# Performance work log

Measured on AMD Instinct MI355X. Metric: run time of the kernel, lower is better.

Reference implementation:

```python
import jax, jax.numpy as jnp
import numpy as np
from jax.ops import segment_sum, segment_max

N, E = 50000, 500000
D_IN, D_H, D_OUT = 128, 256, 40
BN_EPS = 1e-5


def setup_inputs() -> dict:
    key = jax.random.key(0)
    ks = jax.random.split(key, 16)
    g = lambda k, shape, fan: jax.random.normal(k, shape, jnp.float32) * (1.0 / np.sqrt(fan))
    inp = {
        "x": jax.random.normal(ks[0], (N, D_IN), jnp.float32),
        "edge_index": jax.random.randint(ks[1], (2, E), 0, N, jnp.int64),
        # GAT (heads=1)
        "W_gat": g(ks[2], (D_IN, D_H), D_IN),
        "att_src": g(ks[3], (D_H,), D_H),
        "att_dst": g(ks[4], (D_H,), D_H),
        "b_gat": jnp.zeros((D_H,), jnp.float32),
        # GIN MLP
        "W_gin1": g(ks[5], (D_IN, D_H), D_IN),
        "b_gin1": jnp.zeros((D_H,), jnp.float32),
        "W_gin2": g(ks[6], (D_H, D_H), D_H),
        "b_gin2": jnp.zeros((D_H,), jnp.float32),
        # GCN
        "W_gcn": g(ks[7], (D_IN, D_H), D_IN),
        "b_gcn": jnp.zeros((D_H,), jnp.float32),
        # BatchNorm1d(3*hidden)
        "gamma": jnp.ones((3 * D_H,), jnp.float32),
        "beta": jnp.zeros((3 * D_H,), jnp.float32),
        # head
        "W_lin": g(ks[8], (3 * D_H, D_H), 3 * D_H),
        "b_lin": jnp.zeros((D_H,), jnp.float32),
        "W_lin2": g(ks[9], (D_H, D_OUT), D_H),
        "b_lin2": jnp.zeros((D_OUT,), jnp.float32),
    }
    return inp


def _forward(x, edge_index, W_gat, att_src, att_dst, b_gat, W_gin1, b_gin1,
             W_gin2, b_gin2, W_gcn, b_gcn, gamma, beta, W_lin, b_lin, W_lin2, b_lin2):
    n = x.shape[0]
    src, dst = edge_index[0], edge_index[1]
    loop = jnp.arange(n, dtype=src.dtype)
    src_sl = jnp.concatenate([src, loop])  # edges + self-loops (GAT/GCN)
    dst_sl = jnp.concatenate([dst, loop])

    # ---- GATConv (1 head), messages src -> dst, softmax over dst ----
    xs = x @ W_gat                                   # [N, H]
    a = jax.nn.leaky_relu(xs @ att_src, negative_slope=0.2) if False else None
    e = (xs @ att_src)[src_sl] + (xs @ att_dst)[dst_sl]   # [E+N]
    e = jax.nn.leaky_relu(e, negative_slope=0.2)
    m = segment_max(e, dst_sl, num_segments=n)
    w = jnp.exp(e - m[dst_sl])
    denom = segment_sum(w, dst_sl, num_segments=n)
    alpha = w / denom[dst_sl]
    x_gat = segment_sum(alpha[:, None] * xs[src_sl], dst_sl, num_segments=n) + b_gat

    # ---- GINConv (eps=0): MLP(x + sum_neighbors x_j) ----
    agg = segment_sum(x[src], dst, num_segments=n)
    h = x + agg
    x_gin = jax.nn.relu(h @ W_gin1 + b_gin1) @ W_gin2 + b_gin2

    # ---- GCNConv: symmetric normalization with self-loops ----
    deg = segment_sum(jnp.ones_like(dst_sl, dtype=x.dtype), dst_sl, num_segments=n)
    dis = jax.lax.rsqrt(jnp.maximum(deg, 1.0))  # deg >= 1 due to self-loops
    norm = dis[src_sl] * dis[dst_sl]
    xw = x @ W_gcn
    x_gcn = segment_sum(norm[:, None] * xw[src_sl], dst_sl, num_segments=n) + b_gcn

    # ---- concat -> BN (training-mode batch stats) -> ReLU -> MLP head ----
    xc = jnp.concatenate([x_gat, x_gin, x_gcn], axis=1)  # [N, 3H]
    mu = jnp.mean(xc, axis=0)
    var = jnp.mean((xc - mu) ** 2, axis=0)
    xb = (xc - mu) * jax.lax.rsqrt(var + BN_EPS) * gamma + beta
    h2 = jax.nn.relu(jax.nn.relu(xb) @ W_lin + b_lin)
    return h2 @ W_lin2 + b_lin2


def reference(x, edge_index, W_gat, att_src, att_dst, b_gat, W_gin1, b_gin1,
              W_gin2, b_gin2, W_gcn, b_gcn, gamma, beta, W_lin, b_lin, W_lin2, b_lin2):
    return _forward(x, edge_index, W_gat, att_src, att_dst, b_gat, W_gin1, b_gin1,
                    W_gin2, b_gin2, W_gcn, b_gcn, gamma, beta, W_lin, b_lin, W_lin2, b_lin2)
```

## Files before the change

kernel.cpp:

```cpp
#include <hip/hip_runtime.h>
#include <math.h>

#define NN 50000
#define NE 500000

typedef __attribute__((ext_vector_type(8))) short short8;
typedef __attribute__((ext_vector_type(4))) float f32x4;

__device__ __forceinline__ float leaky02(float x) { return x > 0.f ? x : 0.2f * x; }
__device__ __forceinline__ ushort f2b(float f) {
    uint u = __float_as_uint(f);
    u += 0x7fffu + ((u >> 16) & 1u);
    return (ushort)(u >> 16);
}
__device__ __forceinline__ float b2f(ushort h) { return __uint_as_float(((uint)h) << 16); }
__device__ __forceinline__ float b2f_lo(uint w) { return __uint_as_float(w << 16); }
__device__ __forceinline__ float b2f_hi(uint w) { return __uint_as_float(w & 0xffff0000u); }
__device__ __forceinline__ uint pack2(float a, float b) {
    return (uint)f2b(a) | ((uint)f2b(b) << 16);
}

__global__ void mm_wt(const float* __restrict__ W, ushort* __restrict__ Wt, int K, int Nc)
{
    int idx = blockIdx.x * 256 + threadIdx.x;
    if (idx >= K * Nc) return;
    int n = idx / K, k = idx - n * K;
    Wt[idx] = f2b(W[(size_t)k * Nc + n]);
}

__global__ void mm_attvec(const float* __restrict__ W, const float* __restrict__ as_,
                          const float* __restrict__ ad_, float* __restrict__ va, float* __restrict__ vd)
{
    int i = threadIdx.x;
    const float* vec = (i < 128) ? as_ : ad_;
    int k = i & 127;
    float s = 0.f;
    for (int j = 0; j < 256; ++j) s += W[(size_t)k * 256 + j] * vec[j];
    if (i < 128) va[k] = s; else vd[k] = s;
}

__global__ __launch_bounds__(256) void mm_cvt_es(const float* __restrict__ x,
                                                 const float* __restrict__ va, const float* __restrict__ vd,
                                                 ushort* __restrict__ xb,
                                                 float* __restrict__ es, float* __restrict__ ed)
{
    int node = blockIdx.x * 4 + (threadIdx.x >> 6);
    int lane = threadIdx.x & 63;
    if (node >= NN) return;
    float2 xv = *(const float2*)(x + (size_t)node * 128 + lane * 2);
    float2 a = *(const float2*)(va + lane * 2);
    float2 b = *(const float2*)(vd + lane * 2);
    *(uint*)(xb + (size_t)node * 128 + lane * 2) = pack2(xv.x, xv.y);
    float s = xv.x * a.x + xv.y * a.y;
    float d = xv.x * b.x + xv.y * b.y;
    #pragma unroll
    for (int off = 32; off; off >>= 1) {
        s += __shfl_down(s, off);
        d += __shfl_down(d, off);
    }
    if (lane == 0) { es[node] = s; ed[node] = d; }
}

__global__ void mm_count(const int* __restrict__ dst, int* __restrict__ deg)
{
    int e = blockIdx.x * 256 + threadIdx.x;
    if (e >= NE) return;
    atomicAdd(&deg[dst[e]], 1);
}

__global__ __launch_bounds__(256) void mm_scan1(const int* __restrict__ deg, int* __restrict__ part)
{
    __shared__ int red[256];
    int i = blockIdx.x * 256 + threadIdx.x;
    red[threadIdx.x] = (i < NN) ? deg[i] : 0;
    __syncthreads();
    for (int off = 128; off; off >>= 1) {
        if (threadIdx.x < off) red[threadIdx.x] += red[threadIdx.x + off];
        __syncthreads();
    }
    if (threadIdx.x == 0) part[blockIdx.x] = red[0];
}

__global__ __launch_bounds__(256) void mm_scan2(int* __restrict__ part, int nb)
{
    __shared__ int tile[256];
    int t = threadIdx.x;
    int v = (t < nb) ? part[t] : 0;
    tile[t] = v; __syncthreads();
    for (int off = 1; off < 256; off <<= 1) {
        int a = (t >= off) ? tile[t - off] : 0;
        __syncthreads();
        tile[t] += a;
        __syncthreads();
    }
    if (t < nb) part[t] = tile[t] - v;
}

__global__ __launch_bounds__(256) void mm_scan3(const int* __restrict__ deg, const int* __restrict__ part,
                                                int* __restrict__ row_ptr, int* __restrict__ cursor)
{
    __shared__ int tile[256];
    int t = threadIdx.x;
    int i = blockIdx.x * 256 + t;
    int v = (i < NN) ? deg[i] : 0;
    tile[t] = v; __syncthreads();
    for (int off = 1; off < 256; off <<= 1) {
        int a = (t >= off) ? tile[t - off] : 0;
        __syncthreads();
        tile[t] += a;
        __syncthreads();
    }
    if (i < NN) {
        int ex = part[blockIdx.x] + tile[t] - v;
        row_ptr[i] = ex;
        cursor[i] = ex;
    }
    if (i == 0) row_ptr[NN] = NE;
}

__global__ void mm_fill(const int* __restrict__ src, const int* __restrict__ dst,
                        int* __restrict__ cursor, int* __restrict__ csr_src)
{
    int e = blockIdx.x * 256 + threadIdx.x;
    if (e >= NE) return;
    int pos = atomicAdd(&cursor[dst[e]], 1);
    csr_src[pos] = src[e];
}

__global__ void mm_dis(const int* __restrict__ row_ptr, float* __restrict__ dis)
{
    int i = blockIdx.x * 256 + threadIdx.x;
    if (i >= NN) return;
    dis[i] = rsqrtf((float)(row_ptr[i + 1] - row_ptr[i] + 1));
}

__global__ __launch_bounds__(256) void mm_node_agg(
    const int* __restrict__ row_ptr, const int* __restrict__ csr_src,
    const float* __restrict__ es, const float* __restrict__ ed,
    const float* __restrict__ dis,
    const ushort* __restrict__ xb, ushort* __restrict__ aggb)
{
    int d = blockIdx.x * 4 + (threadIdx.x >> 6);
    int lane = threadIdx.x & 63;
    if (d >= NN) return;
    int start = row_ptr[d], end = row_ptr[d + 1];
    float edd = ed[d], disd = dis[d];
    float selfv = leaky02(es[d] + edd);

    int myidx = -1; float myl = -3.0e38f, mynw = 0.f;
    if (start + lane < end) {
        myidx = csr_src[start + lane];
        myl = leaky02(es[myidx] + edd);
        mynw = dis[myidx] * disd;
    }
    float lmax = fmaxf(selfv, myl);
    for (int e = start + 64 + lane; e < end; e += 64)
        lmax = fmaxf(lmax, leaky02(es[csr_src[e]] + edd));
    #pragma unroll
    for (int off = 1; off < 64; off <<= 1) lmax = fmaxf(lmax, __shfl_xor(lmax, off));
    float m = lmax;

    float lsum = (myidx >= 0) ? __expf(myl - m) : 0.f;
    if (lane == 0) lsum += __expf(selfv - m);
    for (int e = start + 64 + lane; e < end; e += 64)
        lsum += __expf(leaky02(es[csr_src[e]] + edd) - m);
    #pragma unroll
    for (int off = 1; off < 64; off <<= 1) lsum += __shfl_xor(lsum, off);
    float inv = 1.f / lsum;
    float myal = __expf(myl - m) * inv;

    float aself = __expf(selfv - m) * inv;
    float d2 = disd * disd;
    uint wself = *(const uint*)(xb + (size_t)d * 128 + lane * 2);
    float x0 = b2f_lo(wself), x1 = b2f_hi(wself);
    float gat0 = aself * x0, gat1 = aself * x1;
    float gin0 = x0, gin1 = x1;
    float gcn0 = d2 * x0, gcn1 = d2 * x1;

    for (int base = start; base < end; base += 64) {
        int cnt = min(64, end - base);
        int bidx; float bal, bnw;
        if (base == start) { bidx = myidx; bal = myal; bnw = mynw; }
        else {
            bidx = -1; bal = 0.f; bnw = 0.f;
            if (base + lane < end) {
                bidx = csr_src[base + lane];
                bal = __expf(leaky02(es[bidx] + edd) - m) * inv;
                bnw = dis[bidx] * disd;
            }
        }
        int j = 0;
        for (; j + 4 <= cnt; j += 4) {
            int   s0 = __shfl(bidx, j),     s1 = __shfl(bidx, j + 1);
            int   s2 = __shfl(bidx, j + 2), s3 = __shfl(bidx, j + 3);
            float a0 = __shfl(bal, j),      a1 = __shfl(bal, j + 1);
            float a2 = __shfl(bal, j + 2),  a3 = __shfl(bal, j + 3);
            float n0 = __shfl(bnw, j),      n1 = __shfl(bnw, j + 1);
            float n2 = __shfl(bnw, j + 2),  n3 = __shfl(bnw, j + 3);
            uint w0 = *(const uint*)(xb + (size_t)s0 * 128 + lane * 2);
            uint w1 = *(const uint*)(xb + (size_t)s1 * 128 + lane * 2);
            uint w2 = *(const uint*)(xb + (size_t)s2 * 128 + lane * 2);
            uint w3 = *(const uint*)(xb + (size_t)s3 * 128 + lane * 2);
            float p0, p1;
            p0 = b2f_lo(w0); p1 = b2f_hi(w0);
            gat0 += a0 * p0; gat1 += a0 * p1; gin0 += p0; gin1 += p1; gcn0 += n0 * p0; gcn1 += n0 * p1;
            p0 = b2f_lo(w1); p1 = b2f_hi(w1);
            gat0 += a1 * p0; gat1 += a1 * p1; gin0 += p0; gin1 += p1; gcn0 += n1 * p0; gcn1 += n1 * p1;
            p0 = b2f_lo(w2); p1 = b2f_hi(w2);
            gat0 += a2 * p0; gat1 += a2 * p1; gin0 += p0; gin1 += p1; gcn0 += n2 * p0; gcn1 += n2 * p1;
            p0 = b2f_lo(w3); p1 = b2f_hi(w3);
            gat0 += a3 * p0; gat1 += a3 * p1; gin0 += p0; gin1 += p1; gcn0 += n3 * p0; gcn1 += n3 * p1;
        }
        for (; j < cnt; ++j) {
            int   s0 = __shfl(bidx, j);
            float a0 = __shfl(bal, j);
            float n0 = __shfl(bnw, j);
            uint w0 = *(const uint*)(xb + (size_t)s0 * 128 + lane * 2);
            float p0 = b2f_lo(w0), p1 = b2f_hi(w0);
            gat0 += a0 * p0; gat1 += a0 * p1; gin0 += p0; gin1 += p1; gcn0 += n0 * p0; gcn1 += n0 * p1;
        }
    }
    ushort* orow = aggb + (size_t)d * 384;
    *(uint*)(orow + lane * 2)       = pack2(gat0, gat1);
    *(uint*)(orow + 128 + lane * 2) = pack2(gin0, gin1);
    *(uint*)(orow + 256 + lane * 2) = pack2(gcn0, gcn1);
}

__global__ __launch_bounds__(256) void mm_gemm_bf(
    const ushort* __restrict__ A, int lda, const ushort* __restrict__ Bt,
    const float* __restrict__ bias,
    ushort* __restrict__ Cb, int ldc,
    int M, int K, int relu)
{
    __shared__ ushort lds[8192];
    const int tid = threadIdx.x;
    const int wave = tid >> 6, lane = tid & 63;
    const int row0 = blockIdx.x * 128;
    const int col0 = blockIdx.y * 128;

    int arow0 = min(row0 + wave * 16 + (lane >> 2), M - 1);
    int arow1 = min(row0 + 64 + wave * 16 + (lane >> 2), M - 1);
    int brow0 = col0 + wave * 16 + (lane >> 2);
    int brow1 = col0 + 64 + wave * 16 + (lane >> 2);
    const ushort* pa0 = A + (size_t)arow0 * lda + (lane & 3) * 8;
    const ushort* pa1 = A + (size_t)arow1 * lda + (lane & 3) * 8;
    const ushort* pb0 = Bt + (size_t)brow0 * K + (lane & 3) * 8;
    const ushort* pb1 = Bt + (size_t)brow1 * K + (lane & 3) * 8;

    ushort* As = lds;
    ushort* Bs = lds + 4096;
    const int wr = (wave >> 1) * 64, wc = (wave & 1) * 64;

    f32x4 zero = {0.f, 0.f, 0.f, 0.f};
    f32x4 acc[4][4];
    #pragma unroll
    for (int m = 0; m < 4; ++m)
        #pragma unroll
        for (int n = 0; n < 4; ++n) acc[m][n] = zero;

    for (int k0 = 0; k0 < K; k0 += 32) {
        __builtin_amdgcn_global_load_lds((const __attribute__((address_space(1))) void*)pa0,
            (__attribute__((address_space(3))) void*)(As + wave * 512), 16, 0, 0);
        __builtin_amdgcn_global_load_lds((const __attribute__((address_space(1))) void*)pa1,
            (__attribute__((address_space(3))) void*)(As + 2048 + wave * 512), 16, 0, 0);
        __builtin_amdgcn_global_load_lds((const __attribute__((address_space(1))) void*)pb0,
            (__attribute__((address_space(3))) void*)(Bs + wave * 512), 16, 0, 0);
        __builtin_amdgcn_global_load_lds((const __attribute__((address_space(1))) void*)pb1,
            (__attribute__((address_space(3))) void*)(Bs + 2048 + wave * 512), 16, 0, 0);
        pa0 += 32; pa1 += 32; pb0 += 32; pb1 += 32;
        __syncthreads();

        short8 a[4], b[4];
        #pragma unroll
        for (int m = 0; m < 4; ++m)
            a[m] = *(const short8*)&As[(wr + m * 16 + (lane & 15)) * 32 + (lane >> 4) * 8];
        #pragma unroll
        for (int n = 0; n < 4; ++n)
            b[n] = *(const short8*)&Bs[(wc + n * 16 + (lane & 15)) * 32 + (lane >> 4) * 8];
        #pragma unroll
        for (int m = 0; m < 4; ++m)
            #pragma unroll
            for (int n = 0; n < 4; ++n)
                acc[m][n] = __builtin_amdgcn_mfma_f32_16x16x32_bf16(a[m], b[n], acc[m][n], 0, 0, 0);
        __syncthreads();
    }

    #pragma unroll
    for (int n = 0; n < 4; ++n) {
        int col = col0 + wc + n * 16 + (lane & 15);
        float bb = bias ? bias[col] : 0.f;
        #pragma unroll
        for (int m = 0; m < 4; ++m) {
            int rb = row0 + wr + m * 16 + (lane >> 4) * 4;
            #pragma unroll
            for (int r = 0; r < 4; ++r) {
                int row = rb + r;
                if (row < M) {
                    float v = acc[m][n][r] + bb;
                    if (relu) v = fmaxf(v, 0.f);
                    Cb[(size_t)row * ldc + col] = f2b(v);
                }
            }
        }
    }
}

__global__ __launch_bounds__(256) void mm_gemm_bn(
    const ushort* __restrict__ A, const ushort* __restrict__ Bt,
    const float* __restrict__ bias,
    const float* __restrict__ sc, const float* __restrict__ sh,
    ushort* __restrict__ Cb, int ldc, int M)
{
    const int K = 768, lda = 768;
    __shared__ ushort lds[8192];
    const int tid = threadIdx.x;
    const int wave = tid >> 6, lane = tid & 63;
    const int row0 = blockIdx.x * 128;
    const int col0 = blockIdx.y * 128;

    int arow0 = min(row0 + wave * 16 + (lane >> 2), M - 1);
    int arow1 = min(row0 + 64 + wave * 16 + (lane >> 2), M - 1);
    int brow0 = col0 + wave * 16 + (lane >> 2);
    int brow1 = col0 + 64 + wave * 16 + (lane >> 2);
    const ushort* pa0 = A + (size_t)arow0 * lda + (lane & 3) * 8;
    const ushort* pa1 = A + (size_t)arow1 * lda + (lane & 3) * 8;
    const ushort* pb0 = Bt + (size_t)brow0 * K + (lane & 3) * 8;
    const ushort* pb1 = Bt + (size_t)brow1 * K + (lane & 3) * 8;

    ushort* As = lds;
    ushort* Bs = lds + 4096;
    const int wr = (wave >> 1) * 64, wc = (wave & 1) * 64;

    f32x4 zero = {0.f, 0.f, 0.f, 0.f};
    f32x4 acc[4][4];
    #pragma unroll
    for (int m = 0; m < 4; ++m)
        #pragma unroll
        for (int n = 0; n < 4; ++n) acc[m][n] = zero;

    for (int k0 = 0; k0 < K; k0 += 32) {
        __builtin_amdgcn_global_load_lds((const __attribute__((address_space(1))) void*)pb0,
            (__attribute__((address_space(3))) void*)(Bs + wave * 512), 16, 0, 0);
        __builtin_amdgcn_global_load_lds((const __attribute__((address_space(1))) void*)pb1,
            (__attribute__((address_space(3))) void*)(Bs + 2048 + wave * 512), 16, 0, 0);
        uint4 w0 = *(const uint4*)pa0;
        uint4 w1 = *(const uint4*)pa1;
        int c = k0 + (lane & 3) * 8;
        float4 sc0 = *(const float4*)(sc + c), sc1 = *(const float4*)(sc + c + 4);
        float4 sh0 = *(const float4*)(sh + c), sh1 = *(const float4*)(sh + c + 4);
        uint o0x = pack2(fmaxf(b2f_lo(w0.x) * sc0.x + sh0.x, 0.f), fmaxf(b2f_hi(w0.x) * sc0.y + sh0.y, 0.f));
        uint o0y = pack2(fmaxf(b2f_lo(w0.y) * sc0.z + sh0.z, 0.f), fmaxf(b2f_hi(w0.y) * sc0.w + sh0.w, 0.f));
        uint o0z = pack2(fmaxf(b2f_lo(w0.z) * sc1.x + sh1.x, 0.f), fmaxf(b2f_hi(w0.z) * sc1.y + sh1.y, 0.f));
        uint o0w = pack2(fmaxf(b2f_lo(w0.w) * sc1.z + sh1.z, 0.f), fmaxf(b2f_hi(w0.w) * sc1.w + sh1.w, 0.f));
        uint o1x = pack2(fmaxf(b2f_lo(w1.x) * sc0.x + sh0.x, 0.f), fmaxf(b2f_hi(w1.x) * sc0.y + sh0.y, 0.f));
        uint o1y = pack2(fmaxf(b2f_lo(w1.y) * sc0.z + sh0.z, 0.f), fmaxf(b2f_hi(w1.y) * sc0.w + sh0.w, 0.f));
        uint o1z = pack2(fmaxf(b2f_lo(w1.z) * sc1.x + sh1.x, 0.f), fmaxf(b2f_hi(w1.z) * sc1.y + sh1.y, 0.f));
        uint o1w = pack2(fmaxf(b2f_lo(w1.w) * sc1.z + sh1.z, 0.f), fmaxf(b2f_hi(w1.w) * sc1.w + sh1.w, 0.f));
        uint4 oa = {o0x, o0y, o0z, o0w};
        uint4 ob = {o1x, o1y, o1z, o1w};
        *(uint4*)(As + wave * 512 + lane * 8) = oa;
        *(uint4*)(As + 2048 + wave * 512 + lane * 8) = ob;
        pa0 += 32; pa1 += 32; pb0 += 32; pb1 += 32;
        __syncthreads();

        short8 a[4], b[4];
        #pragma unroll
        for (int m = 0; m < 4; ++m)
            a[m] = *(const short8*)&As[(wr + m * 16 + (lane & 15)) * 32 + (lane >> 4) * 8];
        #pragma unroll
        for (int n = 0; n < 4; ++n)
            b[n] = *(const short8*)&Bs[(wc + n * 16 + (lane & 15)) * 32 + (lane >> 4) * 8];
        #pragma unroll
        for (int m = 0; m < 4; ++m)
            #pragma unroll
            for (int n = 0; n < 4; ++n)
                acc[m][n] = __builtin_amdgcn_mfma_f32_16x16x32_bf16(a[m], b[n], acc[m][n], 0, 0, 0);
        __syncthreads();
    }

    #pragma unroll
    for (int n = 0; n < 4; ++n) {
        int col = col0 + wc + n * 16 + (lane & 15);
        float bb = bias[col];
        #pragma unroll
        for (int m = 0; m < 4; ++m) {
            int rb = row0 + wr + m * 16 + (lane >> 4) * 4;
            #pragma unroll
            for (int r = 0; r < 4; ++r) {
                int row = rb + r;
                if (row < M)
                    Cb[(size_t)row * ldc + col] = f2b(fmaxf(acc[m][n][r] + bb, 0.f));
            }
        }
    }
}

__global__ __launch_bounds__(384) void mm_bn_partial(const ushort* __restrict__ xcb, float* __restrict__ sums)
{
    int r0 = blockIdx.x * 128;
    int rend = min(r0 + 128, NN);
    int t = threadIdx.x;
    float s0 = 0, q0 = 0, s1 = 0, q1 = 0;
    for (int r = r0; r < rend; ++r) {
        uint w = *(const uint*)(xcb + (size_t)r * 768 + 2 * t);
        float v0 = b2f_lo(w), v1 = b2f_hi(w);
        s0 += v0; q0 += v0 * v0;
        s1 += v1; q1 += v1 * v1;
    }
    unsafeAtomicAdd(&sums[2 * t], s0);
    unsafeAtomicAdd(&sums[2 * t + 1], s1);
    unsafeAtomicAdd(&sums[768 + 2 * t], q0);
    unsafeAtomicAdd(&sums[768 + 2 * t + 1], q1);
}

__global__ void mm_bn_fin(const float* __restrict__ sums, const float* __restrict__ gamma,
                          const float* __restrict__ beta,
                          float* __restrict__ scale, float* __restrict__ shift)
{
    int c = blockIdx.x * 256 + threadIdx.x;
    if (c >= 768) return;
    float inv = 1.f / (float)NN;
    float mu = sums[c] * inv;
    float ex2 = sums[768 + c] * inv;
    float var = fmaxf(ex2 - mu * mu, 0.f);
    float rs = rsqrtf(var + 1e-5f);
    float sc = gamma[c] * rs;
    scale[c] = sc;
    shift[c] = beta[c] - mu * sc;
}

__global__ __launch_bounds__(256) void mm_head2(const ushort* __restrict__ h2b, const float* __restrict__ W2,
                                                const float* __restrict__ b2, float* __restrict__ out)
{
    __shared__ float Ws[256 * 40];
    for (int i = threadIdx.x; i < 256 * 40; i += 256) Ws[i] = W2[i];
    __syncthreads();
    int row = blockIdx.x * 32 + (threadIdx.x >> 3);
    int cg = (threadIdx.x & 7) * 5;
    if (row >= NN) return;
    const ushort* hr = h2b + (size_t)row * 256;
    float acc[5] = {0, 0, 0, 0, 0};
    for (int k = 0; k < 256; k += 8) {
        uint4 w = *(const uint4*)(hr + k);
        float a0 = b2f_lo(w.x), a1 = b2f_hi(w.x), a2 = b2f_lo(w.y), a3 = b2f_hi(w.y);
        float a4 = b2f_lo(w.z), a5 = b2f_hi(w.z), a6 = b2f_lo(w.w), a7 = b2f_hi(w.w);
        #pragma unroll
        for (int j = 0; j < 5; ++j) {
            acc[j] += a0 * Ws[(k + 0) * 40 + cg + j] + a1 * Ws[(k + 1) * 40 + cg + j]
                    + a2 * Ws[(k + 2) * 40 + cg + j] + a3 * Ws[(k + 3) * 40 + cg + j]
                    + a4 * Ws[(k + 4) * 40 + cg + j] + a5 * Ws[(k + 5) * 40 + cg + j]
                    + a6 * Ws[(k + 6) * 40 + cg + j] + a7 * Ws[(k + 7) * 40 + cg + j];
        }
    }
    #pragma unroll
    for (int j = 0; j < 5; ++j) out[(size_t)row * 40 + cg + j] = acc[j] + b2[cg + j];
}

extern "C" void kernel_launch(void* const* d_in, const int* in_sizes, int n_in,
                              void* d_out, int out_size, void* d_ws, size_t ws_size,
                              hipStream_t stream)
{
    const float* x      = (const float*)d_in[0];
    const int*   ei     = (const int*)d_in[1];
    const float* W_gat  = (const float*)d_in[2];
    const float* att_s  = (const float*)d_in[3];
    const float* att_d  = (const float*)d_in[4];
    const float* b_gat  = (const float*)d_in[5];
    const float* W_gin1 = (const float*)d_in[6];
    const float* b_gin1 = (const float*)d_in[7];
    const float* W_gin2 = (const float*)d_in[8];
    const float* b_gin2 = (const float*)d_in[9];
    const float* W_gcn  = (const float*)d_in[10];
    const float* b_gcn  = (const float*)d_in[11];
    const float* gamma  = (const float*)d_in[12];
    const float* beta   = (const float*)d_in[13];
    const float* W_lin  = (const float*)d_in[14];
    const float* b_lin  = (const float*)d_in[15];
    const float* W_lin2 = (const float*)d_in[16];
    const float* b_lin2 = (const float*)d_in[17];
    const int* src = ei;
    const int* dst = ei + NE;
    float* out = (float*)d_out;

    float* ws = (float*)d_ws;
    size_t off = 0;
    ushort* xb      = (ushort*)(ws + off); off += (size_t)NN * 64;
    ushort* aggb    = (ushort*)(ws + off); off += (size_t)NN * 192;
    ushort* hid_b   = (ushort*)(ws + off); off += (size_t)NN * 128;
    ushort* xcb     = (ushort*)(ws + off); off += (size_t)NN * 384;
    float* es       = ws + off; off += NN;
    float* ed       = ws + off; off += NN;
    float* dis      = ws + off; off += NN;
    float* va       = ws + off; off += 128;
    float* vd       = ws + off; off += 128;
    float* bnsum    = ws + off; off += 1536;
    float* bscale   = ws + off; off += 768;
    float* bshift   = ws + off; off += 768;
    ushort* wt_gat  = (ushort*)(ws + off); off += 128 * 256 / 2;
    ushort* wt_gin1 = (ushort*)(ws + off); off += 128 * 256 / 2;
    ushort* wt_gin2 = (ushort*)(ws + off); off += 256 * 256 / 2;
    ushort* wt_gcn  = (ushort*)(ws + off); off += 128 * 256 / 2;
    ushort* wt_lin  = (ushort*)(ws + off); off += 768 * 256 / 2;
    int* part       = (int*)(ws + off); off += 256;
    int* row_ptr    = (int*)(ws + off); off += NN + 1;
    int* cursor     = (int*)(ws + off); off += NN;
    int* csr_src    = (int*)(ws + off); off += NE;

    dim3 blk(256);
    dim3 gemm_grid((NN + 127) / 128, 2);
    const int NB = (NN + 255) / 256;

    mm_wt<<<(128 * 256 + 255) / 256, blk, 0, stream>>>(W_gat, wt_gat, 128, 256);
    mm_wt<<<(128 * 256 + 255) / 256, blk, 0, stream>>>(W_gin1, wt_gin1, 128, 256);
    mm_wt<<<(256 * 256 + 255) / 256, blk, 0, stream>>>(W_gin2, wt_gin2, 256, 256);
    mm_wt<<<(128 * 256 + 255) / 256, blk, 0, stream>>>(W_gcn, wt_gcn, 128, 256);
    mm_wt<<<(768 * 256 + 255) / 256, blk, 0, stream>>>(W_lin, wt_lin, 768, 256);
    mm_attvec<<<1, blk, 0, stream>>>(W_gat, att_s, att_d, va, vd);

    mm_cvt_es<<<(NN + 3) / 4, blk, 0, stream>>>(x, va, vd, xb, es, ed);

    hipMemsetAsync(cursor, 0, NN * sizeof(int), stream);
    mm_count<<<(NE + 255) / 256, blk, 0, stream>>>(dst, cursor);
    mm_scan1<<<NB, blk, 0, stream>>>(cursor, part);
    mm_scan2<<<1, blk, 0, stream>>>(part, NB);
    mm_scan3<<<NB, blk, 0, stream>>>(cursor, part, row_ptr, cursor);
    mm_dis<<<(NN + 255) / 256, blk, 0, stream>>>(row_ptr, dis);
    mm_fill<<<(NE + 255) / 256, blk, 0, stream>>>(src, dst, cursor, csr_src);

    mm_node_agg<<<(NN + 3) / 4, blk, 0, stream>>>(row_ptr, csr_src, es, ed, dis, xb, aggb);

    mm_gemm_bf<<<gemm_grid, blk, 0, stream>>>(aggb,       384, wt_gat,  b_gat,  xcb,       768, NN, 128, 0);
    mm_gemm_bf<<<gemm_grid, blk, 0, stream>>>(aggb + 128, 384, wt_gin1, b_gin1, hid_b,     256, NN, 128, 1);
    mm_gemm_bf<<<gemm_grid, blk, 0, stream>>>(hid_b,      256, wt_gin2, b_gin2, xcb + 256, 768, NN, 256, 0);
    mm_gemm_bf<<<gemm_grid, blk, 0, stream>>>(aggb + 256, 384, wt_gcn,  b_gcn,  xcb + 512, 768, NN, 128, 0);

    hipMemsetAsync(bnsum, 0, 1536 * sizeof(float), stream);
    mm_bn_partial<<<(NN + 127) / 128, dim3(384), 0, stream>>>(xcb, bnsum);
    mm_bn_fin<<<3, blk, 0, stream>>>(bnsum, gamma, beta, bscale, bshift);

    mm_gemm_bn<<<gemm_grid, blk, 0, stream>>>(xcb, wt_lin, b_lin, bscale, bshift, hid_b, 256, NN);
    mm_head2<<<(NN + 31) / 32, blk, 0, stream>>>(hid_b, W_lin2, b_lin2, out);
}
```

Baseline: 430.8 us.

## Double-buffer GEMM LDS tiles and fuse BatchNorm statistics into GEMM epilogue

Both bf16 GEMM kernels now ping-pong between two LDS buffers, loading the next K tile while MFMAs run on the current one, which drops one barrier per iteration. The BN-input GEMM also prefetches its A tile into registers and applies the scale/shift/ReLU after the MFMAs. The separate BatchNorm partial-sum kernel is removed: the GEMM epilogues reduce column sums and sums of squares with shuffles and add them atomically into the stats buffer. This avoids a full re-read of the concatenated feature matrix, at the cost of doubled LDS per block and more atomics. The statistics are taken from the fp32 values before the bf16 rounding, so they differ slightly from before.

```diff
diff --git a/kernel.cpp b/kernel.cpp
--- a/kernel.cpp
+++ b/kernel.cpp
@@ -228,11 +228,11 @@
 
 __global__ __launch_bounds__(256) void mm_gemm_bf(
     const ushort* __restrict__ A, int lda, const ushort* __restrict__ Bt,
-    const float* __restrict__ bias,
+    const float* __restrict__ bias, float* __restrict__ stats,
     ushort* __restrict__ Cb, int ldc,
     int M, int K, int relu)
 {
-    __shared__ ushort lds[8192];
+    __shared__ ushort lds[16384];
     const int tid = threadIdx.x;
     const int wave = tid >> 6, lane = tid & 63;
     const int row0 = blockIdx.x * 128;
@@ -246,9 +246,6 @@
     const ushort* pa1 = A + (size_t)arow1 * lda + (lane & 3) * 8;
     const ushort* pb0 = Bt + (size_t)brow0 * K + (lane & 3) * 8;
     const ushort* pb1 = Bt + (size_t)brow1 * K + (lane & 3) * 8;
-
-    ushort* As = lds;
-    ushort* Bs = lds + 4096;
     const int wr = (wave >> 1) * 64, wc = (wave & 1) * 64;
 
     f32x4 zero = {0.f, 0.f, 0.f, 0.f};
@@ -258,18 +255,27 @@
         #pragma unroll
         for (int n = 0; n < 4; ++n) acc[m][n] = zero;
 
-    for (int k0 = 0; k0 < K; k0 += 32) {
-        __builtin_amdgcn_global_load_lds((const __attribute__((address_space(1))) void*)pa0,
-            (__attribute__((address_space(3))) void*)(As + wave * 512), 16, 0, 0);
-        __builtin_amdgcn_global_load_lds((const __attribute__((address_space(1))) void*)pa1,
-            (__attribute__((address_space(3))) void*)(As + 2048 + wave * 512), 16, 0, 0);
-        __builtin_amdgcn_global_load_lds((const __attribute__((address_space(1))) void*)pb0,
-            (__attribute__((address_space(3))) void*)(Bs + wave * 512), 16, 0, 0);
-        __builtin_amdgcn_global_load_lds((const __attribute__((address_space(1))) void*)pb1,
-            (__attribute__((address_space(3))) void*)(Bs + 2048 + wave * 512), 16, 0, 0);
-        pa0 += 32; pa1 += 32; pb0 += 32; pb1 += 32;
-        __syncthreads();
-
+    const int nt = K >> 5;
+
+#define STAGE_BF(bufi) { \
+    ushort* Lb = lds + (bufi) * 8192; \
+    __builtin_amdgcn_global_load_lds((const __attribute__((address_space(1))) void*)pa0, \
+        (__attribute__((address_space(3))) void*)(Lb + wave * 512), 16, 0, 0); \
+    __builtin_amdgcn_global_load_lds((const __attribute__((address_space(1))) void*)pa1, \
+        (__attribute__((address_space(3))) void*)(Lb + 2048 + wave * 512), 16, 0, 0); \
+    __builtin_amdgcn_global_load_lds((const __attribute__((address_space(1))) void*)pb0, \
+        (__attribute__((address_space(3))) void*)(Lb + 4096 + wave * 512), 16, 0, 0); \
+    __builtin_amdgcn_global_load_lds((const __attribute__((address_space(1))) void*)pb1, \
+        (__attribute__((address_space(3))) void*)(Lb + 6144 + wave * 512), 16, 0, 0); \
+    pa0 += 32; pa1 += 32; pb0 += 32; pb1 += 32; }
+
+    STAGE_BF(0);
+    __syncthreads();
+    for (int t = 0; t < nt; ++t) {
+        int cur = t & 1;
+        if (t + 1 < nt) STAGE_BF(cur ^ 1);
+        const ushort* As = lds + cur * 8192;
+        const ushort* Bs = As + 4096;
         short8 a[4], b[4];
         #pragma unroll
         for (int m = 0; m < 4; ++m)
@@ -282,13 +288,15 @@
             #pragma unroll
             for (int n = 0; n < 4; ++n)
                 acc[m][n] = __builtin_amdgcn_mfma_f32_16x16x32_bf16(a[m], b[n], acc[m][n], 0, 0, 0);
-        __syncthreads();
-    }
+        if (t + 1 < nt) __syncthreads();
+    }
+#undef STAGE_BF
 
     #pragma unroll
     for (int n = 0; n < 4; ++n) {
         int col = col0 + wc + n * 16 + (lane & 15);
         float bb = bias ? bias[col] : 0.f;
+        float s_acc = 0.f, q_acc = 0.f;
         #pragma unroll
         for (int m = 0; m < 4; ++m) {
             int rb = row0 + wr + m * 16 + (lane >> 4) * 4;
@@ -299,10 +307,32 @@
                     float v = acc[m][n][r] + bb;
                     if (relu) v = fmaxf(v, 0.f);
                     Cb[(size_t)row * ldc + col] = f2b(v);
+                    s_acc += v; q_acc += v * v;
                 }
             }
         }
-    }
+        if (stats) {
+            s_acc += __shfl_xor(s_acc, 16); q_acc += __shfl_xor(q_acc, 16);
+            s_acc += __shfl_xor(s_acc, 32); q_acc += __shfl_xor(q_acc, 32);
+            if (lane < 16) {
+                unsafeAtomicAdd(&stats[col], s_acc);
+                unsafeAtomicAdd(&stats[768 + col], q_acc);
+            }
+        }
+    }
+}
+
+__device__ __forceinline__ uint4 bn_relu_pack(uint4 w, const float* __restrict__ sc,
+                                              const float* __restrict__ sh, int c)
+{
+    float4 sc0 = *(const float4*)(sc + c), sc1 = *(const float4*)(sc + c + 4);
+    float4 sh0 = *(const float4*)(sh + c), sh1 = *(const float4*)(sh + c + 4);
+    uint4 o;
+    o.x = pack2(fmaxf(b2f_lo(w.x) * sc0.x + sh0.x, 0.f), fmaxf(b2f_hi(w.x) * sc0.y + sh0.y, 0.f));
+    o.y = pack2(fmaxf(b2f_lo(w.y) * sc0.z + sh0.z, 0.f), fmaxf(b2f_hi(w.y) * sc0.w + sh0.w, 0.f));
+    o.z = pack2(fmaxf(b2f_lo(w.z) * sc1.x + sh1.x, 0.f), fmaxf(b2f_hi(w.z) * sc1.y + sh1.y, 0.f));
+    o.w = pack2(fmaxf(b2f_lo(w.w) * sc1.z + sh1.z, 0.f), fmaxf(b2f_hi(w.w) * sc1.w + sh1.w, 0.f));
+    return o;
 }
 
 __global__ __launch_bounds__(256) void mm_gemm_bn(
@@ -312,7 +342,7 @@
     ushort* __restrict__ Cb, int ldc, int M)
 {
     const int K = 768, lda = 768;
-    __shared__ ushort lds[8192];
+    __shared__ ushort lds[16384];
     const int tid = threadIdx.x;
     const int wave = tid >> 6, lane = tid & 63;
     const int row0 = blockIdx.x * 128;
@@ -326,9 +356,6 @@
     const ushort* pa1 = A + (size_t)arow1 * lda + (lane & 3) * 8;
     const ushort* pb0 = Bt + (size_t)brow0 * K + (lane & 3) * 8;
     const ushort* pb1 = Bt + (size_t)brow1 * K + (lane & 3) * 8;
-
-    ushort* As = lds;
-    ushort* Bs = lds + 4096;
     const int wr = (wave >> 1) * 64, wc = (wave & 1) * 64;
 
     f32x4 zero = {0.f, 0.f, 0.f, 0.f};
@@ -338,31 +365,40 @@
         #pragma unroll
         for (int n = 0; n < 4; ++n) acc[m][n] = zero;
 
-    for (int k0 = 0; k0 < K; k0 += 32) {
-        __builtin_amdgcn_global_load_lds((const __attribute__((address_space(1))) void*)pb0,
-            (__attribute__((address_space(3))) void*)(Bs + wave * 512), 16, 0, 0);
-        __builtin_amdgcn_global_load_lds((const __attribute__((address_space(1))) void*)pb1,
-            (__attribute__((address_space(3))) void*)(Bs + 2048 + wave * 512), 16, 0, 0);
-        uint4 w0 = *(const uint4*)pa0;
-        uint4 w1 = *(const uint4*)pa1;
-        int c = k0 + (lane & 3) * 8;
-        float4 sc0 = *(const float4*)(sc + c), sc1 = *(const float4*)(sc + c + 4);
-        float4 sh0 = *(const float4*)(sh + c), sh1 = *(const float4*)(sh + c + 4);
-        uint o0x = pack2(fmaxf(b2f_lo(w0.x) * sc0.x + sh0.x, 0.f), fmaxf(b2f_hi(w0.x) * sc0.y + sh0.y, 0.f));
-        uint o0y = pack2(fmaxf(b2f_lo(w0.y) * sc0.z + sh0.z, 0.f), fmaxf(b2f_hi(w0.y) * sc0.w + sh0.w, 0.f));
-        uint o0z = pack2(fmaxf(b2f_lo(w0.z) * sc1.x + sh1.x, 0.f), fmaxf(b2f_hi(w0.z) * sc1.y + sh1.y, 0.f));
-        uint o0w = pack2(fmaxf(b2f_lo(w0.w) * sc1.z + sh1.z, 0.f), fmaxf(b2f_hi(w0.w) * sc1.w + sh1.w, 0.f));
-        uint o1x = pack2(fmaxf(b2f_lo(w1.x) * sc0.x + sh0.x, 0.f), fmaxf(b2f_hi(w1.x) * sc0.y + sh0.y, 0.f));
-        uint o1y = pack2(fmaxf(b2f_lo(w1.y) * sc0.z + sh0.z, 0.f), fmaxf(b2f_hi(w1.y) * sc0.w + sh0.w, 0.f));
-        uint o1z = pack2(fmaxf(b2f_lo(w1.z) * sc1.x + sh1.x, 0.f), fmaxf(b2f_hi(w1.z) * sc1.y + sh1.y, 0.f));
-        uint o1w = pack2(fmaxf(b2f_lo(w1.w) * sc1.z + sh1.z, 0.f), fmaxf(b2f_hi(w1.w) * sc1.w + sh1.w, 0.f));
-        uint4 oa = {o0x, o0y, o0z, o0w};
-        uint4 ob = {o1x, o1y, o1z, o1w};
-        *(uint4*)(As + wave * 512 + lane * 8) = oa;
-        *(uint4*)(As + 2048 + wave * 512 + lane * 8) = ob;
-        pa0 += 32; pa1 += 32; pb0 += 32; pb1 += 32;
-        __syncthreads();
-
+    const int nt = K >> 5;
+
+#define STAGE_B(bufi) { \
+    ushort* Lb = lds + (bufi) * 8192; \
+    __builtin_amdgcn_global_load_lds((const __attribute__((address_space(1))) void*)pb0, \
+        (__attribute__((address_space(3))) void*)(Lb + 4096 + wave * 512), 16, 0, 0); \
+    __builtin_amdgcn_global_load_lds((const __attribute__((address_space(1))) void*)pb1, \
+        (__attribute__((address_space(3))) void*)(Lb + 6144 + wave * 512), 16, 0, 0); \
+    pb0 += 32; pb1 += 32; }
+
+    {
+        STAGE_B(0);
+        uint4 w0 = *(const uint4*)pa0; uint4 w1 = *(const uint4*)pa1;
+        pa0 += 32; pa1 += 32;
+        int c = (lane & 3) * 8;
+        uint4 oa = bn_relu_pack(w0, sc, sh, c);
+        uint4 ob = bn_relu_pack(w1, sc, sh, c);
+        *(uint4*)(lds + wave * 512 + lane * 8) = oa;
+        *(uint4*)(lds + 2048 + wave * 512 + lane * 8) = ob;
+    }
+    __syncthreads();
+
+    for (int t = 0; t < nt; ++t) {
+        int cur = t & 1;
+        uint4 w0n, w1n; int cn = 0;
+        bool more = (t + 1 < nt);
+        if (more) {
+            STAGE_B(cur ^ 1);
+            w0n = *(const uint4*)pa0; w1n = *(const uint4*)pa1;
+            pa0 += 32; pa1 += 32;
+            cn = (t + 1) * 32 + (lane & 3) * 8;
+        }
+        const ushort* As = lds + cur * 8192;
+        const ushort* Bs = As + 4096;
         short8 a[4], b[4];
         #pragma unroll
         for (int m = 0; m < 4; ++m)
@@ -375,8 +411,16 @@
             #pragma unroll
             for (int n = 0; n < 4; ++n)
                 acc[m][n] = __builtin_amdgcn_mfma_f32_16x16x32_bf16(a[m], b[n], acc[m][n], 0, 0, 0);
-        __syncthreads();
-    }
+        if (more) {
+            ushort* Ln = lds + (cur ^ 1) * 8192;
+            uint4 oa = bn_relu_pack(w0n, sc, sh, cn);
+            uint4 ob = bn_relu_pack(w1n, sc, sh, cn);
+            *(uint4*)(Ln + wave * 512 + lane * 8) = oa;
+            *(uint4*)(Ln + 2048 + wave * 512 + lane * 8) = ob;
+            __syncthreads();
+        }
+    }
+#undef STAGE_B
 
     #pragma unroll
     for (int n = 0; n < 4; ++n) {
@@ -393,24 +437,6 @@
             }
         }
     }
-}
-
-__global__ __launch_bounds__(384) void mm_bn_partial(const ushort* __restrict__ xcb, float* __restrict__ sums)
-{
-    int r0 = blockIdx.x * 128;
-    int rend = min(r0 + 128, NN);
-    int t = threadIdx.x;
-    float s0 = 0, q0 = 0, s1 = 0, q1 = 0;
-    for (int r = r0; r < rend; ++r) {
-        uint w = *(const uint*)(xcb + (size_t)r * 768 + 2 * t);
-        float v0 = b2f_lo(w), v1 = b2f_hi(w);
-        s0 += v0; q0 += v0 * v0;
-        s1 += v1; q1 += v1 * v1;
-    }
-    unsafeAtomicAdd(&sums[2 * t], s0);
-    unsafeAtomicAdd(&sums[2 * t + 1], s1);
-    unsafeAtomicAdd(&sums[768 + 2 * t], q0);
-    unsafeAtomicAdd(&sums[768 + 2 * t + 1], q1);
 }
 
 __global__ void mm_bn_fin(const float* __restrict__ sums, const float* __restrict__ gamma,
@@ -510,6 +536,9 @@
     dim3 gemm_grid((NN + 127) / 128, 2);
     const int NB = (NN + 255) / 256;
 
+    hipMemsetAsync(bnsum, 0, 1536 * sizeof(float), stream);
+    hipMemsetAsync(cursor, 0, NN * sizeof(int), stream);
+
     mm_wt<<<(128 * 256 + 255) / 256, blk, 0, stream>>>(W_gat, wt_gat, 128, 256);
     mm_wt<<<(128 * 256 + 255) / 256, blk, 0, stream>>>(W_gin1, wt_gin1, 128, 256);
     mm_wt<<<(256 * 256 + 255) / 256, blk, 0, stream>>>(W_gin2, wt_gin2, 256, 256);
@@ -519,7 +548,6 @@
 
     mm_cvt_es<<<(NN + 3) / 4, blk, 0, stream>>>(x, va, vd, xb, es, ed);
 
-    hipMemsetAsync(cursor, 0, NN * sizeof(int), stream);
     mm_count<<<(NE + 255) / 256, blk, 0, stream>>>(dst, cursor);
     mm_scan1<<<NB, blk, 0, stream>>>(cursor, part);
     mm_scan2<<<1, blk, 0, stream>>>(part, NB);
@@ -529,13 +557,11 @@
 
     mm_node_agg<<<(NN + 3) / 4, blk, 0, stream>>>(row_ptr, csr_src, es, ed, dis, xb, aggb);
 
-    mm_gemm_bf<<<gemm_grid, blk, 0, stream>>>(aggb,       384, wt_gat,  b_gat,  xcb,       768, NN, 128, 0);
-    mm_gemm_bf<<<gemm_grid, blk, 0, stream>>>(aggb + 128, 384, wt_gin1, b_gin1, hid_b,     256, NN, 128, 1);
-    mm_gemm_bf<<<gemm_grid, blk, 0, stream>>>(hid_b,      256, wt_gin2, b_gin2, xcb + 256, 768, NN, 256, 0);
-    mm_gemm_bf<<<gemm_grid, blk, 0, stream>>>(aggb + 256, 384, wt_gcn,  b_gcn,  xcb + 512, 768, NN, 128, 0);
-
-    hipMemsetAsync(bnsum, 0, 1536 * sizeof(float), stream);
-    mm_bn_partial<<<(NN + 127) / 128, dim3(384), 0, stream>>>(xcb, bnsum);
+    mm_gemm_bf<<<gemm_grid, blk, 0, stream>>>(aggb,       384, wt_gat,  b_gat,  bnsum,       xcb,       768, NN, 128, 0);
+    mm_gemm_bf<<<gemm_grid, blk, 0, stream>>>(aggb + 128, 384, wt_gin1, b_gin1, nullptr,     hid_b,     256, NN, 128, 1);
+    mm_gemm_bf<<<gemm_grid, blk, 0, stream>>>(hid_b,      256, wt_gin2, b_gin2, bnsum + 256, xcb + 256, 768, NN, 256, 0);
+    mm_gemm_bf<<<gemm_grid, blk, 0, stream>>>(aggb + 256, 384, wt_gcn,  b_gcn,  bnsum + 512, xcb + 512, 768, NN, 128, 0);
+
     mm_bn_fin<<<3, blk, 0, stream>>>(bnsum, gamma, beta, bscale, bshift);
 
     mm_gemm_bn<<<gemm_grid, blk, 0, stream>>>(xcb, wt_lin, b_lin, bscale, bshift, hid_b, 256, NN);
```

Result: faster. 419.2 us (-2.7%).
